# Kernel tuning notes

Measured on AMD Instinct MI355X. Metric: run time of the kernel, lower is better.

The kernel has to match this reference:

```python
import jax, jax.numpy as jnp
import numpy as np

EPS = 1e-12
NUM_HEADS = 16
FEATURE_DIM = 16
HEAD_DIM = 64


def setup_inputs() -> dict:
    key = jax.random.key(0)
    k1, k2, k3, k4, k5 = jax.random.split(key, 5)
    b, l, d_model = 2, 2048, 1024
    scale = 0.02
    return {
        "hidden_states": jax.random.normal(k1, (b, l, d_model), jnp.float32),
        "Wq": jax.random.normal(k2, (FEATURE_DIM * NUM_HEADS, d_model), jnp.float32) * scale,
        "Wk": jax.random.normal(k3, (FEATURE_DIM * NUM_HEADS, d_model), jnp.float32) * scale,
        "Wv": jax.random.normal(k4, (NUM_HEADS * HEAD_DIM, d_model), jnp.float32) * scale,
        "Wo": jax.random.normal(k5, (d_model, NUM_HEADS * HEAD_DIM), jnp.float32) * scale,
    }


def reference(hidden_states, Wq, Wk, Wv, Wo):
    b, l, d_model = hidden_states.shape
    h, fd, hd = NUM_HEADS, FEATURE_DIM, HEAD_DIM
    # projections (no bias), split heads: (b, h, l, dim)
    q = (hidden_states @ Wq.T).reshape(b, l, h, fd).transpose(0, 2, 1, 3)
    k = (hidden_states @ Wk.T).reshape(b, l, h, fd).transpose(0, 2, 1, 3)
    v = (hidden_states @ Wv.T).reshape(b, l, h, hd).transpose(0, 2, 1, 3)
    # feature map is identity (default FeatureMap)
    # quadratic causal linear attention
    A_qk = jnp.einsum("bhnd,bhmd->bhnm", q, k)  # [b,h,l,l]
    A_qk = jnp.tril(A_qk)
    y = jnp.einsum("bhnm,bhme->bhne", A_qk, v)  # [b,h,l,hd]
    # denominator: q . cumsum(k)
    z = 1.0 / (jnp.einsum("bhld,bhld->bhl", q, jnp.cumsum(k, axis=2)) + EPS)
    y = y * z[..., None]
    # merge heads and output projection
    y = y.transpose(0, 2, 1, 3).reshape(b, l, h * hd)
    return y @ Wo.T
```

## Files before the change

### kernel.cpp

```cpp
#include <hip/hip_runtime.h>
#include <hip/hip_bf16.h>

#define NH 16
#define FD 16
#define HD 64
#define BATCH 2
#define SEQ 2048
#define DM 1024
#define ROWS (BATCH * SEQ)
#define CHUNK 128
#define NCH (SEQ / CHUNK)
#define NBH (BATCH * NH)

typedef __hip_bfloat16 bf16;
typedef __attribute__((ext_vector_type(8))) short short8;
typedef __attribute__((ext_vector_type(4))) float f32x4;

__device__ inline float bfbits(unsigned int h) {
  union { unsigned int u; float f; } c; c.u = h << 16; return c.f;
}
__device__ inline unsigned short f2bf(float x) {
  bf16 h = __float2bfloat16(x);
  return *(unsigned short*)&h;
}

__device__ inline void load8(const void* src, size_t idx, int isf32, float* out) {
  if (isf32) {
    const float* p = (const float*)src + idx;
    float4 a = *(const float4*)p;
    float4 b = *(const float4*)(p + 4);
    out[0] = a.x; out[1] = a.y; out[2] = a.z; out[3] = a.w;
    out[4] = b.x; out[5] = b.y; out[6] = b.z; out[7] = b.w;
  } else {
    const uint4 w = *(const uint4*)((const unsigned short*)src + idx);
    out[0] = bfbits(w.x & 0xffffu); out[1] = bfbits(w.x >> 16);
    out[2] = bfbits(w.y & 0xffffu); out[3] = bfbits(w.y >> 16);
    out[4] = bfbits(w.z & 0xffffu); out[5] = bfbits(w.z >> 16);
    out[6] = bfbits(w.w & 0xffffu); out[7] = bfbits(w.w >> 16);
  }
}

__device__ inline void gload16(const void* g, void* l) {
  __builtin_amdgcn_global_load_lds(
      (const __attribute__((address_space(1))) unsigned int*)g,
      (__attribute__((address_space(3))) unsigned int*)l, 16, 0, 0);
}

__global__ __launch_bounds__(256) void detect_dtype(const unsigned int* __restrict__ w,
                                                    int* __restrict__ flag) {
  __shared__ int red[256];
  int cnt = 0;
  for (int i = threadIdx.x; i < 4096; i += 256) {
    unsigned int e = (w[i] >> 7) & 0xFFu;
    cnt += (e >= 0x90u) ? 1 : 0;
  }
  red[threadIdx.x] = cnt;
  __syncthreads();
  for (int s = 128; s > 0; s >>= 1) {
    if (threadIdx.x < s) red[threadIdx.x] += red[threadIdx.x + s];
    __syncthreads();
  }
  if (threadIdx.x == 0) *flag = (red[0] > 64) ? 1 : 0;
}

__global__ __launch_bounds__(256) void gemm_qk4(const void* __restrict__ A,
                                                const void* __restrict__ Wq,
                                                const void* __restrict__ Wk,
                                                const int* __restrict__ flagp,
                                                float* __restrict__ qf,
                                                float* __restrict__ kf) {
  const int isf32 = *flagp;
  __shared__ float As[128 * 36];
  __shared__ float Bs[64 * 36];
  const int tid = threadIdx.x;
  const int m0 = blockIdx.x * 128;
  const int isK = blockIdx.y >> 2;
  const int n0 = (blockIdx.y & 3) * 64;
  const void* B = isK ? Wk : Wq;
  float* C = isK ? kf : qf;
  const int tx = tid & 15, ty = tid >> 4;
  const int lmA = tid >> 1, lcA = (tid & 1) * 16;
  const int lmB = tid >> 2, lcB = (tid & 3) * 8;
  double dacc[8][4];
#pragma unroll
  for (int i = 0; i < 8; ++i)
#pragma unroll
    for (int n = 0; n < 4; ++n) dacc[i][n] = 0.0;

  float av[16], bv[8];
  load8(A, (size_t)(m0 + lmA) * DM + lcA, isf32, &av[0]);
  load8(A, (size_t)(m0 + lmA) * DM + lcA + 8, isf32, &av[8]);
  load8(B, (size_t)(n0 + lmB) * DM + lcB, isf32, bv);

  for (int kt = 0; kt < DM; kt += 32) {
    __syncthreads();
    *(float4*)&As[lmA * 36 + lcA] = *(float4*)&av[0];
    *(float4*)&As[lmA * 36 + lcA + 4] = *(float4*)&av[4];
    *(float4*)&As[lmA * 36 + lcA + 8] = *(float4*)&av[8];
    *(float4*)&As[lmA * 36 + lcA + 12] = *(float4*)&av[12];
    *(float4*)&Bs[lmB * 36 + lcB] = *(float4*)&bv[0];
    *(float4*)&Bs[lmB * 36 + lcB + 4] = *(float4*)&bv[4];
    __syncthreads();
    if (kt + 32 < DM) {
      load8(A, (size_t)(m0 + lmA) * DM + kt + 32 + lcA, isf32, &av[0]);
      load8(A, (size_t)(m0 + lmA) * DM + kt + 32 + lcA + 8, isf32, &av[8]);
      load8(B, (size_t)(n0 + lmB) * DM + kt + 32 + lcB, isf32, bv);
    }
    for (int kk = 0; kk < 32; kk += 4) {
      float4 ar[8], br[4];
#pragma unroll
      for (int i = 0; i < 8; ++i) ar[i] = *(const float4*)&As[(tx + 16 * i) * 36 + kk];
#pragma unroll
      for (int n = 0; n < 4; ++n) br[n] = *(const float4*)&Bs[(ty * 4 + n) * 36 + kk];
      float facc[8][4] = {};
#pragma unroll
      for (int j = 0; j < 4; ++j) {
#pragma unroll
        for (int i = 0; i < 8; ++i) {
          float a = ((const float*)&ar[i])[j];
#pragma unroll
          for (int n = 0; n < 4; ++n)
            facc[i][n] += a * ((const float*)&br[n])[j];
        }
      }
#pragma unroll
      for (int i = 0; i < 8; ++i)
#pragma unroll
        for (int n = 0; n < 4; ++n) dacc[i][n] += (double)facc[i][n];
    }
  }
#pragma unroll
  for (int i = 0; i < 8; ++i) {
    int row = m0 + tx + 16 * i;
    float4 o;
    o.x = (float)dacc[i][0]; o.y = (float)dacc[i][1];
    o.z = (float)dacc[i][2]; o.w = (float)dacc[i][3];
    *(float4*)&C[(size_t)row * 256 + n0 + ty * 4] = o;
  }
}

template <int MODE>
__global__ __launch_bounds__(256) void gemm_mfma(const void* __restrict__ Ap,
                                                 const void* __restrict__ Bp,
                                                 const int* __restrict__ flagp,
                                                 void* __restrict__ Cp) {
  const int isf32 = *flagp;
  const int aF32 = (MODE == 0) ? isf32 : 0;
  const int bF32 = isf32;
  __shared__ unsigned short As[128 * 32];
  __shared__ unsigned short Bs[64 * 32];
  const int tid = threadIdx.x;
  const int wave = tid >> 6, lane = tid & 63;
  const int m0 = blockIdx.x * 128, n0 = blockIdx.y * 64;
  const int lrow = lane >> 2, lch = (lane & 3) * 8;
  const int wm = wave >> 1, wn = wave & 1;
  const int mlane = lane & 15, kgrp = lane >> 4;
  const unsigned short* Ab = (const unsigned short*)Ap;
  const unsigned short* Bb = (const unsigned short*)Bp;
  f32x4 acc[4][2];
#pragma unroll
  for (int t = 0; t < 4; ++t)
#pragma unroll
    for (int u = 0; u < 2; ++u) acc[t][u] = (f32x4){0.f, 0.f, 0.f, 0.f};

  for (int k0 = 0; k0 < DM; k0 += 32) {
    __syncthreads();
    if (!aF32) {
      const int r0 = wave * 32;
#pragma unroll
      for (int j = 0; j < 2; ++j) {
        const void* g = Ab + (size_t)(m0 + r0 + j * 16 + lrow) * DM + k0 + lch;
        gload16(g, &As[(r0 + j * 16) * 32]);
      }
    } else {
      for (int c = tid; c < 512; c += 256) {
        int r = c >> 2, cc = (c & 3) * 8;
        float v8[8];
        load8(Ap, (size_t)(m0 + r) * DM + k0 + cc, 1, v8);
        unsigned int w[4];
#pragma unroll
        for (int g2 = 0; g2 < 4; ++g2)
          w[g2] = (unsigned)f2bf(v8[2 * g2]) | ((unsigned)f2bf(v8[2 * g2 + 1]) << 16);
        *(uint4*)&As[r * 32 + cc] = *(uint4*)w;
      }
    }
    if (!bF32) {
      const void* g = Bb + (size_t)(n0 + wave * 16 + lrow) * DM + k0 + lch;
      gload16(g, &Bs[(wave * 16) * 32]);
    } else {
      {
        int c = tid;
        int r = c >> 2, cc = (c & 3) * 8;
        float v8[8];
        load8(Bp, (size_t)(n0 + r) * DM + k0 + cc, 1, v8);
        unsigned int w[4];
#pragma unroll
        for (int g2 = 0; g2 < 4; ++g2)
          w[g2] = (unsigned)f2bf(v8[2 * g2]) | ((unsigned)f2bf(v8[2 * g2 + 1]) << 16);
        *(uint4*)&Bs[r * 32 + cc] = *(uint4*)w;
      }
    }
    __syncthreads();

    short8 af[4], bfr[2];
#pragma unroll
    for (int t = 0; t < 4; ++t)
      af[t] = *(const short8*)&As[(wm * 64 + t * 16 + mlane) * 32 + kgrp * 8];
#pragma unroll
    for (int u = 0; u < 2; ++u)
      bfr[u] = *(const short8*)&Bs[(wn * 32 + u * 16 + mlane) * 32 + kgrp * 8];
#pragma unroll
    for (int t = 0; t < 4; ++t)
#pragma unroll
      for (int u = 0; u < 2; ++u)
        acc[t][u] = __builtin_amdgcn_mfma_f32_16x16x32_bf16(af[t], bfr[u], acc[t][u], 0, 0, 0);
  }

#pragma unroll
  for (int t = 0; t < 4; ++t)
#pragma unroll
    for (int u = 0; u < 2; ++u)
#pragma unroll
      for (int r = 0; r < 4; ++r) {
        int row = m0 + wm * 64 + t * 16 + kgrp * 4 + r;
        int col = n0 + wn * 32 + u * 16 + mlane;
        float v = acc[t][u][r];
        if (MODE == 0) {
          ((unsigned short*)Cp)[(size_t)row * DM + col] = f2bf(v);
        } else if (isf32) {
          ((float*)Cp)[(size_t)row * DM + col] = v;
        } else {
          ((unsigned short*)Cp)[(size_t)row * DM + col] = f2bf(v);
        }
      }
}

__global__ __launch_bounds__(256) void attn_intra(const float* __restrict__ qf,
                                                  const float* __restrict__ kf,
                                                  const unsigned short* __restrict__ vfb,
                                                  unsigned short* __restrict__ yib,
                                                  float* __restrict__ Sc,
                                                  double* __restrict__ Kc) {
  __shared__ float qc[CHUNK][20];
  __shared__ float kc[CHUNK][20];
  __shared__ float vc[CHUNK][68];
  const int bh = blockIdx.x >> 4;
  const int c = blockIdx.x & 15;
  const int b = bh >> 4, h = bh & 15;
  const int bl = c * CHUNK;
  const int tid = threadIdx.x;

  for (int idx = tid; idx < CHUNK * FD / 4; idx += 256) {
    int r = idx >> 2, f4 = (idx & 3) * 4;
    size_t g = ((size_t)(b * SEQ + bl + r)) * (NH * FD) + h * FD + f4;
    *(float4*)&qc[r][f4] = *(const float4*)&qf[g];
    *(float4*)&kc[r][f4] = *(const float4*)&kf[g];
  }
  for (int idx = tid; idx < CHUNK * HD / 8; idx += 256) {
    int r = idx >> 3, e8 = (idx & 7) * 8;
    uint4 w = *(const uint4*)&vfb[((size_t)(b * SEQ + bl + r)) * (NH * HD) + h * HD + e8];
    vc[r][e8 + 0] = bfbits(w.x & 0xffffu); vc[r][e8 + 1] = bfbits(w.x >> 16);
    vc[r][e8 + 2] = bfbits(w.y & 0xffffu); vc[r][e8 + 3] = bfbits(w.y >> 16);
    vc[r][e8 + 4] = bfbits(w.z & 0xffffu); vc[r][e8 + 5] = bfbits(w.z >> 16);
    vc[r][e8 + 6] = bfbits(w.w & 0xffffu); vc[r][e8 + 7] = bfbits(w.w >> 16);
  }
  __syncthreads();

  const int p = tid >> 2;
  const int n0 = 2 * p, n1 = 2 * p + 1;
  const int e0 = (tid & 3) * 16;
  float q0r[16], q1r[16];
#pragma unroll
  for (int d = 0; d < 16; ++d) { q0r[d] = qc[n0][d]; q1r[d] = qc[n1][d]; }
  float y0[16], y1[16];
#pragma unroll
  for (int e = 0; e < 16; ++e) { y0[e] = 0.f; y1[e] = 0.f; }

  for (int m = 0; m <= n1; ++m) {
    float kd[16], vv[16];
#pragma unroll
    for (int d = 0; d < 16; ++d) kd[d] = kc[m][d];
#pragma unroll
    for (int e = 0; e < 16; ++e) vv[e] = vc[m][e0 + e];
    float d0 = 0.f, d1 = 0.f;
#pragma unroll
    for (int d = 0; d < 16; ++d) { d0 += q0r[d] * kd[d]; d1 += q1r[d] * kd[d]; }
    if (m > n0) d0 = 0.f;
#pragma unroll
    for (int e = 0; e < 16; ++e) { y0[e] += d0 * vv[e]; y1[e] += d1 * vv[e]; }
  }
  const size_t ybase = (size_t)bh * SEQ + bl;
  {
    unsigned int w[4];
#pragma unroll
    for (int g = 0; g < 4; ++g)
      w[g] = (unsigned)f2bf(y0[2 * g]) | ((unsigned)f2bf(y0[2 * g + 1]) << 16);
    *(uint4*)&yib[(ybase + n0) * HD + e0] = *(uint4*)w;
#pragma unroll
    for (int g = 0; g < 4; ++g)
      w[g] = (unsigned)f2bf(y0[8 + 2 * g]) | ((unsigned)f2bf(y0[9 + 2 * g]) << 16);
    *(uint4*)&yib[(ybase + n0) * HD + e0 + 8] = *(uint4*)w;
#pragma unroll
    for (int g = 0; g < 4; ++g)
      w[g] = (unsigned)f2bf(y1[2 * g]) | ((unsigned)f2bf(y1[2 * g + 1]) << 16);
    *(uint4*)&yib[(ybase + n1) * HD + e0] = *(uint4*)w;
#pragma unroll
    for (int g = 0; g < 4; ++g)
      w[g] = (unsigned)f2bf(y1[8 + 2 * g]) | ((unsigned)f2bf(y1[9 + 2 * g]) << 16);
    *(uint4*)&yib[(ybase + n1) * HD + e0 + 8] = *(uint4*)w;
  }

  float* Scp = Sc + ((size_t)bh * NCH + c) * (FD * HD);
  for (int idx = tid; idx < FD * HD; idx += 256) {
    int d = idx >> 6, e = idx & 63;
    float s = 0.f;
    for (int m = 0; m < CHUNK; ++m) s += kc[m][d] * vc[m][e];
    Scp[idx] = s;
  }
  if (tid < FD) {
    double ks = 0.0;
    for (int m = 0; m < CHUNK; ++m) ks += (double)kc[m][tid];
    Kc[((size_t)bh * NCH + c) * FD + tid] = ks;
  }
}

__global__ __launch_bounds__(256) void scan_states(float* __restrict__ Sc,
                                                   double* __restrict__ Kc) {
  const int bh = blockIdx.x;
  const int tid = threadIdx.x;
  float4 acc = make_float4(0.f, 0.f, 0.f, 0.f);
  size_t base = (size_t)bh * NCH * (FD * HD) + (size_t)tid * 4;
  for (int c = 0; c < NCH; ++c) {
    float4* p = (float4*)(Sc + base + (size_t)c * (FD * HD));
    float4 v = *p;
    *p = acc;
    acc.x += v.x; acc.y += v.y; acc.z += v.z; acc.w += v.w;
  }
  if (tid < FD) {
    double a = 0.0;
    for (int c = 0; c < NCH; ++c) {
      size_t i = ((size_t)bh * NCH + c) * FD + tid;
      double t = Kc[i];
      Kc[i] = a;
      a += t;
    }
  }
}

__global__ __launch_bounds__(256) void attn_finish(const float* __restrict__ qf,
                                                   const float* __restrict__ kf,
                                                   const unsigned short* __restrict__ yib,
                                                   const float* __restrict__ Sc,
                                                   const double* __restrict__ Kc,
                                                   unsigned short* __restrict__ yob) {
  __shared__ float qc[CHUNK][20];
  __shared__ float kc[CHUNK][20];
  __shared__ float Sp[FD][HD];
  __shared__ double cs[CHUNK][17];
  __shared__ double zl[CHUNK];
  __shared__ double ksp[FD];
  const int bh = blockIdx.x >> 4;
  const int c = blockIdx.x & 15;
  const int b = bh >> 4, h = bh & 15;
  const int bl = c * CHUNK;
  const int tid = threadIdx.x;

  for (int idx = tid; idx < CHUNK * FD / 4; idx += 256) {
    int r = idx >> 2, f4 = (idx & 3) * 4;
    size_t g = ((size_t)(b * SEQ + bl + r)) * (NH * FD) + h * FD + f4;
    *(float4*)&qc[r][f4] = *(const float4*)&qf[g];
    *(float4*)&kc[r][f4] = *(const float4*)&kf[g];
  }
  const float* Scp = Sc + ((size_t)bh * NCH + c) * (FD * HD);
  for (int idx = tid; idx < FD * HD / 4; idx += 256) {
    int d = idx >> 4, e4 = (idx & 15) * 4;
    *(float4*)&Sp[d][e4] = *(const float4*)&Scp[(size_t)d * HD + e4];
  }
  if (tid < FD) ksp[tid] = Kc[((size_t)bh * NCH + c) * FD + tid];
  __syncthreads();

  if (tid < FD) {
    double run = ksp[tid];
    for (int m = 0; m < CHUNK; ++m) {
      run += (double)kc[m][tid];
      cs[m][tid] = run;
    }
  }
  __syncthreads();
  if (tid < CHUNK) {
    double dn = 0.0;
#pragma unroll
    for (int d = 0; d < 16; ++d) dn += (double)qc[tid][d] * cs[tid][d];
    zl[tid] = 1.0 / (dn + 1e-12);
  }
  __syncthreads();

  for (int idx = tid; idx < CHUNK * HD / 8; idx += 256) {
    int n = idx >> 3, e8 = (idx & 7) * 8;
    uint4 w = *(const uint4*)&yib[((size_t)bh * SEQ + bl + n) * HD + e8];
    float yv[8] = {bfbits(w.x & 0xffffu), bfbits(w.x >> 16),
                   bfbits(w.y & 0xffffu), bfbits(w.y >> 16),
                   bfbits(w.z & 0xffffu), bfbits(w.z >> 16),
                   bfbits(w.w & 0xffffu), bfbits(w.w >> 16)};
    double z = zl[n];
    unsigned int o[4];
#pragma unroll
    for (int jp = 0; jp < 4; ++jp) {
      int e = e8 + 2 * jp;
      float i0 = 0.f, i1 = 0.f;
#pragma unroll
      for (int d = 0; d < 16; ++d) {
        i0 += qc[n][d] * Sp[d][e];
        i1 += qc[n][d] * Sp[d][e + 1];
      }
      float r0 = (float)(((double)(yv[2 * jp] + i0)) * z);
      float r1 = (float)(((double)(yv[2 * jp + 1] + i1)) * z);
      o[jp] = (unsigned)f2bf(r0) | ((unsigned)f2bf(r1) << 16);
    }
    *(uint4*)&yob[((size_t)(b * SEQ + bl + n)) * (NH * HD) + h * HD + e8] = *(uint4*)o;
  }
}

extern "C" void kernel_launch(void* const* d_in, const int* in_sizes, int n_in,
                              void* d_out, int out_size, void* d_ws, size_t ws_size,
                              hipStream_t stream) {
  (void)in_sizes; (void)n_in; (void)out_size; (void)ws_size;
  const void* hs = d_in[0];
  const void* Wq = d_in[1];
  const void* Wk = d_in[2];
  const void* Wv = d_in[3];
  const void* Wo = d_in[4];

  char* ws = (char*)d_ws;
  float* qf = (float*)(ws);
  float* kf = (float*)(ws + (4u << 20));
  unsigned short* vfb = (unsigned short*)(ws + (8u << 20));
  unsigned short* yob = vfb;
  unsigned short* yib = (unsigned short*)(ws + (16u << 20));
  float* Sc = (float*)(ws + (24u << 20));
  double* Kc = (double*)(ws + (26u << 20));
  int* flag = (int*)(ws + (26u << 20) + 65536);

  detect_dtype<<<1, 256, 0, stream>>>((const unsigned int*)hs, flag);
  gemm_qk4<<<dim3(ROWS / 128, 8), 256, 0, stream>>>(hs, Wq, Wk, flag, qf, kf);
  gemm_mfma<0><<<dim3(ROWS / 128, 1024 / 64), 256, 0, stream>>>(hs, Wv, flag, vfb);
  attn_intra<<<NBH * NCH, 256, 0, stream>>>(qf, kf, vfb, yib, Sc, Kc);
  scan_states<<<NBH, 256, 0, stream>>>(Sc, Kc);
  attn_finish<<<NBH * NCH, 256, 0, stream>>>(qf, kf, yib, Sc, Kc, yob);
  gemm_mfma<1><<<dim3(ROWS / 128, 1024 / 64), 256, 0, stream>>>(yob, Wo, flag, d_out);
}
```

Before: 319.9 us.

## Split-K the Q/K projection GEMM across two half-blocks with smaller M tiles

The Q/K projection kernel now uses 64-row tiles instead of 128, doubling the grid. Each block splits the K dimension between two 128-thread halves, each with its own shared-memory tiles. The partial double-precision accumulators are combined through shared memory before the store. This targets low occupancy and wave count in the fp64-accumulating GEMM, at the cost of an extra reduction and more shared memory per block.

```diff
diff --git a/kernel.cpp b/kernel.cpp
--- a/kernel.cpp
+++ b/kernel.cpp
@@ -63,53 +63,62 @@
   if (threadIdx.x == 0) *flag = (red[0] > 64) ? 1 : 0;
 }
 
-__global__ __launch_bounds__(256) void gemm_qk4(const void* __restrict__ A,
-                                                const void* __restrict__ Wq,
-                                                const void* __restrict__ Wk,
-                                                const int* __restrict__ flagp,
-                                                float* __restrict__ qf,
-                                                float* __restrict__ kf) {
+__global__ __launch_bounds__(256, 2) void gemm_qk5(const void* __restrict__ A,
+                                                   const void* __restrict__ Wq,
+                                                   const void* __restrict__ Wk,
+                                                   const int* __restrict__ flagp,
+                                                   float* __restrict__ qf,
+                                                   float* __restrict__ kf) {
   const int isf32 = *flagp;
-  __shared__ float As[128 * 36];
-  __shared__ float Bs[64 * 36];
+  __shared__ float smem[9216];
   const int tid = threadIdx.x;
-  const int m0 = blockIdx.x * 128;
+  const int h = tid >> 7;
+  const int ltid = tid & 127;
+  float* As = smem + h * 2304;
+  float* Bs = smem + 4608 + h * 2304;
+  const int m0 = blockIdx.x * 64;
   const int isK = blockIdx.y >> 2;
   const int n0 = (blockIdx.y & 3) * 64;
   const void* B = isK ? Wk : Wq;
   float* C = isK ? kf : qf;
-  const int tx = tid & 15, ty = tid >> 4;
-  const int lmA = tid >> 1, lcA = (tid & 1) * 16;
-  const int lmB = tid >> 2, lcB = (tid & 3) * 8;
+  const int tx = ltid & 7;
+  const int ty = ltid >> 3;
+  const int lm = ltid >> 1, lcH = (ltid & 1) * 16;
+  const int kbase = h * 512;
   double dacc[8][4];
 #pragma unroll
   for (int i = 0; i < 8; ++i)
 #pragma unroll
     for (int n = 0; n < 4; ++n) dacc[i][n] = 0.0;
 
-  float av[16], bv[8];
-  load8(A, (size_t)(m0 + lmA) * DM + lcA, isf32, &av[0]);
-  load8(A, (size_t)(m0 + lmA) * DM + lcA + 8, isf32, &av[8]);
-  load8(B, (size_t)(n0 + lmB) * DM + lcB, isf32, bv);
-
-  for (int kt = 0; kt < DM; kt += 32) {
+  float av[16], bv[16];
+  load8(A, (size_t)(m0 + lm) * DM + kbase + lcH, isf32, &av[0]);
+  load8(A, (size_t)(m0 + lm) * DM + kbase + lcH + 8, isf32, &av[8]);
+  load8(B, (size_t)(n0 + lm) * DM + kbase + lcH, isf32, &bv[0]);
+  load8(B, (size_t)(n0 + lm) * DM + kbase + lcH + 8, isf32, &bv[8]);
+
+  for (int t = 0; t < 16; ++t) {
     __syncthreads();
-    *(float4*)&As[lmA * 36 + lcA] = *(float4*)&av[0];
-    *(float4*)&As[lmA * 36 + lcA + 4] = *(float4*)&av[4];
-    *(float4*)&As[lmA * 36 + lcA + 8] = *(float4*)&av[8];
-    *(float4*)&As[lmA * 36 + lcA + 12] = *(float4*)&av[12];
-    *(float4*)&Bs[lmB * 36 + lcB] = *(float4*)&bv[0];
-    *(float4*)&Bs[lmB * 36 + lcB + 4] = *(float4*)&bv[4];
+    *(float4*)&As[lm * 36 + lcH] = *(float4*)&av[0];
+    *(float4*)&As[lm * 36 + lcH + 4] = *(float4*)&av[4];
+    *(float4*)&As[lm * 36 + lcH + 8] = *(float4*)&av[8];
+    *(float4*)&As[lm * 36 + lcH + 12] = *(float4*)&av[12];
+    *(float4*)&Bs[lm * 36 + lcH] = *(float4*)&bv[0];
+    *(float4*)&Bs[lm * 36 + lcH + 4] = *(float4*)&bv[4];
+    *(float4*)&Bs[lm * 36 + lcH + 8] = *(float4*)&bv[8];
+    *(float4*)&Bs[lm * 36 + lcH + 12] = *(float4*)&bv[12];
     __syncthreads();
-    if (kt + 32 < DM) {
-      load8(A, (size_t)(m0 + lmA) * DM + kt + 32 + lcA, isf32, &av[0]);
-      load8(A, (size_t)(m0 + lmA) * DM + kt + 32 + lcA + 8, isf32, &av[8]);
-      load8(B, (size_t)(n0 + lmB) * DM + kt + 32 + lcB, isf32, bv);
+    if (t < 15) {
+      int kt = kbase + (t + 1) * 32;
+      load8(A, (size_t)(m0 + lm) * DM + kt + lcH, isf32, &av[0]);
+      load8(A, (size_t)(m0 + lm) * DM + kt + lcH + 8, isf32, &av[8]);
+      load8(B, (size_t)(n0 + lm) * DM + kt + lcH, isf32, &bv[0]);
+      load8(B, (size_t)(n0 + lm) * DM + kt + lcH + 8, isf32, &bv[8]);
     }
     for (int kk = 0; kk < 32; kk += 4) {
       float4 ar[8], br[4];
 #pragma unroll
-      for (int i = 0; i < 8; ++i) ar[i] = *(const float4*)&As[(tx + 16 * i) * 36 + kk];
+      for (int i = 0; i < 8; ++i) ar[i] = *(const float4*)&As[(tx + 8 * i) * 36 + kk];
 #pragma unroll
       for (int n = 0; n < 4; ++n) br[n] = *(const float4*)&Bs[(ty * 4 + n) * 36 + kk];
       float facc[8][4] = {};
@@ -129,13 +138,27 @@
         for (int n = 0; n < 4; ++n) dacc[i][n] += (double)facc[i][n];
     }
   }
-#pragma unroll
-  for (int i = 0; i < 8; ++i) {
-    int row = m0 + tx + 16 * i;
-    float4 o;
-    o.x = (float)dacc[i][0]; o.y = (float)dacc[i][1];
-    o.z = (float)dacc[i][2]; o.w = (float)dacc[i][3];
-    *(float4*)&C[(size_t)row * 256 + n0 + ty * 4] = o;
+
+  double* dbl = (double*)smem;
+  __syncthreads();
+  if (h == 1) {
+#pragma unroll
+    for (int i = 0; i < 8; ++i)
+#pragma unroll
+      for (int n = 0; n < 4; ++n) dbl[ltid * 32 + i * 4 + n] = dacc[i][n];
+  }
+  __syncthreads();
+  if (h == 0) {
+#pragma unroll
+    for (int i = 0; i < 8; ++i) {
+#pragma unroll
+      for (int n = 0; n < 4; ++n) dacc[i][n] += dbl[ltid * 32 + i * 4 + n];
+      int row = m0 + tx + 8 * i;
+      float4 o;
+      o.x = (float)dacc[i][0]; o.y = (float)dacc[i][1];
+      o.z = (float)dacc[i][2]; o.w = (float)dacc[i][3];
+      *(float4*)&C[(size_t)row * 256 + n0 + ty * 4] = o;
+    }
   }
 }
 
@@ -442,7 +465,7 @@
   int* flag = (int*)(ws + (26u << 20) + 65536);
 
   detect_dtype<<<1, 256, 0, stream>>>((const unsigned int*)hs, flag);
-  gemm_qk4<<<dim3(ROWS / 128, 8), 256, 0, stream>>>(hs, Wq, Wk, flag, qf, kf);
+  gemm_qk5<<<dim3(ROWS / 64, 8), 256, 0, stream>>>(hs, Wq, Wk, flag, qf, kf);
   gemm_mfma<0><<<dim3(ROWS / 128, 1024 / 64), 256, 0, stream>>>(hs, Wv, flag, vfb);
   attn_intra<<<NBH * NCH, 256, 0, stream>>>(qf, kf, vfb, yib, Sc, Kc);
   scan_states<<<NBH, 256, 0, stream>>>(Sc, Kc);
```

New measurement: 298.6 us. 6.7% less time.
